# Kernel tuning notes

Hardware: AMD Instinct MI355X
Metric: run time of the kernel (lower is better)

Reference implementation:

```python
import jax, jax.numpy as jnp
import numpy as np

DIM = 128
N = 16          # num_nodes
B = 8           # batch size
H = 4096        # MLP hidden width
SLOPE = 0.01    # LeakyReLU default negative slope
PI_ITERS = 50   # fixed-iteration power iteration (max_error=1e-5 regime)


def setup_inputs() -> dict:
    key = jax.random.key(0)
    ks = jax.random.split(key, 12)
    w = lambda k, shape: jax.random.normal(k, shape, jnp.float32) * 0.02
    return {
        "nodes_embeddings": jax.random.normal(ks[0], (B, N, DIM), jnp.float32),
        "graphs_embeddings": jax.random.normal(ks[1], (B, DIM), jnp.float32),
        "Ts": jax.random.uniform(ks[2], (B, N, N), jnp.float32),
        "W1": w(ks[3], (2 * DIM, H)), "b1": jnp.zeros((H,), jnp.float32),
        "W2": w(ks[4], (H, H)),       "b2": jnp.zeros((H,), jnp.float32),
        "W3": w(ks[5], (H, H)),       "b3": jnp.zeros((H,), jnp.float32),
        "W4": w(ks[6], (H, N * N)),   "b4": jnp.zeros((N * N,), jnp.float32),
    }


def _mlp(x, W1, b1, W2, b2, W3, b3, W4, b4):
    # Linear -> LeakyReLU -> (Dropout=eval identity), x3, then Linear -> LeakyReLU -> Sigmoid
    h = jax.nn.leaky_relu(x @ W1 + b1, SLOPE)
    h = jax.nn.leaky_relu(h @ W2 + b2, SLOPE)
    h = jax.nn.leaky_relu(h @ W3 + b3, SLOPE)
    return jax.nn.sigmoid(jax.nn.leaky_relu(h @ W4 + b4, SLOPE))


def _power_iteration(A):
    # A: (..., n, n), entries > 0 (sigmoid outputs) -> dominant (Perron) eigenvector.
    v0 = jnp.ones(A.shape[:-1], A.dtype)
    def step(v, _):
        w = jnp.einsum('...ij,...j->...i', A, v)
        v = w / jnp.linalg.norm(w, axis=-1, keepdims=True)
        return v, None
    v, _ = jax.lax.scan(step, v0, None, length=PI_ITERS)
    return v


def reference(nodes_embeddings, graphs_embeddings, Ts, W1, b1, W2, b2, W3, b3, W4, b4):
    Bn, Nn, D = nodes_embeddings.shape
    P = Nn * Nn
    pair = jnp.arange(P)
    s_ids = pair // Nn  # outer loop index s
    t_ids = pair % Nn   # inner loop index t

    embT = jnp.transpose(nodes_embeddings, (1, 0, 2))      # (N, B, D)
    s_all = embT[s_ids]                                    # (P, B, D)
    t_all = embT[t_ids]                                    # (P, B, D)
    # Faithful to torch.stack([s, t]).view(batch, 2*dim): a flat reinterpretation,
    # NOT a per-row concat. stack axis=1 -> (P, 2, B, D) then reshape -> (P, B, 2D).
    x = jnp.stack([s_all, t_all], axis=1).reshape(P, Bn, 2 * D)

    pol = _mlp(x.reshape(P * Bn, 2 * D), W1, b1, W2, b2, W3, b3, W4, b4)
    pol = pol.reshape(P, Bn, Nn, Nn)                       # predecessor prob matrices

    vec = _power_iteration(pol)                            # (P, B, N)
    v_src = vec[pair, :, s_ids]                            # (P, B) eigenvector[src]
    T_pair = jnp.transpose(Ts.reshape(Bn, P), (1, 0))      # (P, B), pair order s*N+t

    contrib = vec / v_src[:, :, None] * T_pair[:, :, None]  # (P, B, N)
    return jnp.sum(contrib, axis=0)                         # (B, N) == Cs
```

## Files before the change

kernel.cpp:

```cpp
#include <hip/hip_runtime.h>

typedef unsigned short u16;
typedef unsigned int u32;
typedef __attribute__((ext_vector_type(8))) short short8;
typedef __attribute__((ext_vector_type(4))) float f32x4;

__device__ __forceinline__ u16 f2bf(float f) {
    unsigned u = __float_as_uint(f);
    return (u16)((u + 0x7FFFu + ((u >> 16) & 1u)) >> 16);
}
__device__ __forceinline__ u32 pack2(float a, float b) {
    return ((u32)f2bf(b) << 16) | (u32)f2bf(a);
}

#define ROR1 0x121
#define ROR2 0x122
#define ROR4 0x124
#define ROR8 0x128
template<int C> __device__ __forceinline__ float dppf(float x) {
    int i = __float_as_int(x);
    return __int_as_float(__builtin_amdgcn_update_dpp(i, i, C, 0xF, 0xF, false));
}
template<int C> __device__ __forceinline__ int dppi(int x) {
    return __builtin_amdgcn_update_dpp(x, x, C, 0xF, 0xF, false);
}

template<int SRC, int EPI>
__global__ __launch_bounds__(256, 1) void k_gemm(
    const u16* __restrict__ A, const float* __restrict__ emb,
    const float* __restrict__ W, const float* __restrict__ bias,
    float* __restrict__ Cp, u16* __restrict__ Ho, float* __restrict__ Po,
    int N, int kchunk)
{
    __shared__ __align__(16) u16 Alds[64][40];
    __shared__ __align__(16) u32 Wlds[16 * 132];
    int tid = threadIdx.x;
    int wv = tid >> 6, lane = tid & 63, c = lane & 15, g = lane >> 4;
    int c0 = blockIdx.x * 128;
    int k0 = blockIdx.y * kchunk;
    int nit = kchunk >> 5;

    int ar = tid >> 2, aseg = tid & 3;
    int kp = tid >> 4, cbase = (tid & 15) * 8;

    f32x4 acc[8];
    #pragma unroll
    for (int n = 0; n < 8; ++n) acc[n] = (f32x4){0.f, 0.f, 0.f, 0.f};

    uint4 av;
    float4 q0, q1, q2, q3;

    {
        if (SRC == 0) {
            av = *(const uint4*)(A + (size_t)ar * 4096 + k0 + aseg * 8);
        } else {
            int e0 = aseg * 8;
            int b = 2 * (ar & 3) + (e0 >> 7), d = e0 & 127;
            const float4* s = (const float4*)(emb + (b * 16 + (ar >> 2)) * 128 + d);
            float4 f0 = s[0], f1 = s[1];
            av.x = pack2(f0.x, f0.y); av.y = pack2(f0.z, f0.w);
            av.z = pack2(f1.x, f1.y); av.w = pack2(f1.z, f1.w);
        }
        const float* s0 = W + (size_t)(k0 + 2 * kp) * N + c0 + cbase;
        q0 = ((const float4*)s0)[0]; q1 = ((const float4*)s0)[1];
        const float* s1 = s0 + N;
        q2 = ((const float4*)s1)[0]; q3 = ((const float4*)s1)[1];
    }

    for (int it = 0; it < nit; ++it) {
        *(uint4*)&Alds[ar][aseg * 8] = av;
        {
            uint4 w0, w1;
            w0.x = pack2(q0.x, q2.x); w0.y = pack2(q0.y, q2.y);
            w0.z = pack2(q0.z, q2.z); w0.w = pack2(q0.w, q2.w);
            w1.x = pack2(q1.x, q3.x); w1.y = pack2(q1.y, q3.y);
            w1.z = pack2(q1.z, q3.z); w1.w = pack2(q1.w, q3.w);
            uint4* wd = (uint4*)&Wlds[kp * 132 + cbase];
            wd[0] = w0; wd[1] = w1;
        }
        __syncthreads();

        if (it + 1 < nit) {
            int kc = (it + 1) * 32;
            if (SRC == 0) {
                av = *(const uint4*)(A + (size_t)ar * 4096 + k0 + kc + aseg * 8);
            } else {
                int e0 = kc + aseg * 8;
                int b = 2 * (ar & 3) + (e0 >> 7), d = e0 & 127;
                const float4* s = (const float4*)(emb + (b * 16 + (ar >> 2)) * 128 + d);
                float4 f0 = s[0], f1 = s[1];
                av.x = pack2(f0.x, f0.y); av.y = pack2(f0.z, f0.w);
                av.z = pack2(f1.x, f1.y); av.w = pack2(f1.z, f1.w);
            }
            const float* s0 = W + (size_t)(k0 + kc + 2 * kp) * N + c0 + cbase;
            q0 = ((const float4*)s0)[0]; q1 = ((const float4*)s0)[1];
            const float* s1 = s0 + N;
            q2 = ((const float4*)s1)[0]; q3 = ((const float4*)s1)[1];
        }

        short8 a8 = *(const short8*)&Alds[wv * 16 + c][g * 8];
        #pragma unroll
        for (int n = 0; n < 8; ++n) {
            int base = n * 16 + c;
            union { u32 u[4]; short8 s; } bb;
            bb.u[0] = Wlds[(g * 4 + 0) * 132 + base];
            bb.u[1] = Wlds[(g * 4 + 1) * 132 + base];
            bb.u[2] = Wlds[(g * 4 + 2) * 132 + base];
            bb.u[3] = Wlds[(g * 4 + 3) * 132 + base];
            acc[n] = __builtin_amdgcn_mfma_f32_16x16x32_bf16(a8, bb.s, acc[n], 0, 0, 0);
        }
        __syncthreads();
    }

    #pragma unroll
    for (int n = 0; n < 8; ++n) {
        #pragma unroll
        for (int rr = 0; rr < 4; ++rr) {
            int grow = wv * 16 + g * 4 + rr;
            int gcol = c0 + n * 16 + c;
            float v = acc[n][rr];
            if (EPI == 0) {
                Cp[(size_t)blockIdx.y * 64 * N + (size_t)grow * N + gcol] = v;
            } else {
                v += bias[gcol];
                v = (v >= 0.f) ? v : 0.01f * v;
                if (EPI == 1) Ho[(size_t)grow * N + gcol] = f2bf(v);
                else          Po[(size_t)grow * N + gcol] = 1.0f / (1.0f + __expf(-v));
            }
        }
    }
}

__global__ void k_reduce(const float* __restrict__ Cp, const float* __restrict__ bias,
                         u16* __restrict__ Hb, float* __restrict__ Pf,
                         int N, int ksplit, int mode)
{
    int idx = blockIdx.x * 256 + threadIdx.x;
    int col = idx & (N - 1);
    float s = bias[col];
    for (int k = 0; k < ksplit; ++k) s += Cp[(size_t)k * 64 * N + idx];
    float a = (s >= 0.f) ? s : 0.01f * s;
    if (mode == 0) Hb[idx] = f2bf(a);
    else           Pf[idx] = 1.0f / (1.0f + __expf(-a));
}

__global__ __launch_bounds__(1024) void k_power_out(
    const float* __restrict__ pol,
    const float* __restrict__ Ts,
    float* __restrict__ out)
{
    __shared__ float pol_lds[16384];
    __shared__ float w_lds[64][16];
    __shared__ float Ts_lds[2048];
    __shared__ float Cmat[8][16];

    int tid = threadIdx.x;
    int m = tid >> 4, r = tid & 15;

    {
        const float4* p4 = (const float4*)(pol + tid * 16);
        float4* q4 = (float4*)&pol_lds[tid * 16];
        q4[0] = p4[0]; q4[1] = p4[1]; q4[2] = p4[2]; q4[3] = p4[3];
    }
    Ts_lds[tid] = Ts[tid];
    Ts_lds[tid + 1024] = Ts[tid + 1024];
    __syncthreads();

    float Mr[8], Ms[8];
    {
        int mb = m * 256 + r * 16;
        int idx = r;
        #pragma unroll
        for (int k = 0; k < 8; ++k) { Mr[k] = pol_lds[mb + idx]; idx = dppi<ROR1>(idx); }
        #pragma unroll
        for (int k = 0; k < 8; ++k) { Ms[k] = pol_lds[mb + idx]; idx = dppi<ROR1>(idx); }
    }

    float v = 1.0f;
    #pragma unroll 1
    for (int it = 0; it < 50; ++it) {
        float va = v, vb = dppf<ROR8>(v);
        float w = 0.f, w2 = 0.f;
        #pragma unroll
        for (int k = 0; k < 8; ++k) {
            w  = fmaf(Mr[k], va, w);
            w2 = fmaf(Ms[k], vb, w2);
            if (k < 7) { va = dppf<ROR1>(va); vb = dppf<ROR1>(vb); }
        }
        w += w2;
        if ((it & 7) == 7) {
            float s = w;
            s += dppf<ROR8>(s); s += dppf<ROR4>(s);
            s += dppf<ROR2>(s); s += dppf<ROR1>(s);
            w *= 1.0f / s;
        }
        v = w;
    }
    w_lds[m][r] = v;
    __syncthreads();

    if (tid < 128) {
        int b = tid >> 4, x = tid & 15;
        float s = 0.f;
        if (b < 4) {
            const float* row = &Ts_lds[(b * 16 + x) * 16];
            #pragma unroll
            for (int t = 0; t < 16; ++t) s += row[t];
        } else {
            int j = b - 4;
            #pragma unroll
            for (int si = 0; si < 16; ++si)
                s += Ts_lds[(b * 16 + si) * 16 + x] / w_lds[x * 4 + j][si];
        }
        Cmat[b][x] = s;
    }
    __syncthreads();

    if (tid < 128) {
        int b = tid >> 4, n = tid & 15;
        float o = 0.f;
        if (b < 4) {
            #pragma unroll
            for (int si = 0; si < 16; ++si) {
                const float* wr = w_lds[si * 4 + b];
                o += wr[n] / wr[si] * Cmat[b][si];
            }
        } else {
            int j = b - 4;
            #pragma unroll
            for (int t = 0; t < 16; ++t)
                o += w_lds[t * 4 + j][n] * Cmat[b][t];
        }
        out[b * 16 + n] = o;
    }
}

extern "C" void kernel_launch(void* const* d_in, const int* in_sizes, int n_in,
                              void* d_out, int out_size, void* d_ws, size_t ws_size,
                              hipStream_t stream)
{
    const float* emb = (const float*)d_in[0];
    const float* Ts  = (const float*)d_in[2];
    const float* W1  = (const float*)d_in[3];  const float* b1 = (const float*)d_in[4];
    const float* W2  = (const float*)d_in[5];  const float* b2 = (const float*)d_in[6];
    const float* W3  = (const float*)d_in[7];  const float* b3 = (const float*)d_in[8];
    const float* W4  = (const float*)d_in[9];  const float* b4 = (const float*)d_in[10];
    float* outp = (float*)d_out;

    char* ws = (char*)d_ws;
    u16*   Ha  = (u16*)(ws + 0);
    u16*   Hb  = (u16*)(ws + 524288);
    float* pol = (float*)(ws + 1048576);
    float* Cp  = (float*)(ws + 1114112);

    k_gemm<1, 1><<<dim3(32, 1), 256, 0, stream>>>(
        nullptr, emb, W1, b1, nullptr, Ha, nullptr, 4096, 256);

    k_gemm<0, 0><<<dim3(32, 8), 256, 0, stream>>>(
        Ha, nullptr, W2, nullptr, Cp, nullptr, nullptr, 4096, 512);
    k_reduce<<<1024, 256, 0, stream>>>(Cp, b2, Hb, nullptr, 4096, 8, 0);

    k_gemm<0, 0><<<dim3(32, 8), 256, 0, stream>>>(
        Hb, nullptr, W3, nullptr, Cp, nullptr, nullptr, 4096, 512);
    k_reduce<<<1024, 256, 0, stream>>>(Cp, b3, Ha, nullptr, 4096, 8, 0);

    k_gemm<0, 0><<<dim3(2, 32), 256, 0, stream>>>(
        Ha, nullptr, W4, nullptr, Cp, nullptr, nullptr, 256, 128);
    k_reduce<<<64, 256, 0, stream>>>(Cp, b4, nullptr, pol, 256, 32, 1);

    k_power_out<<<1, 1024, 0, stream>>>(pol, Ts, outp);

    (void)in_sizes; (void)n_in; (void)out_size; (void)ws_size;
}
```

Measured before the change: 85.79 us.

## Double-buffer GEMM global prefetch and raise split-K to sixteen chunks

Rewrites the GEMM main loop into a two-deep register prefetch (A and B sets), so loads for step it+2 are in flight while step it computes. It also relaxes launch bounds to allow two blocks per CU and doubles the split-K factor for the two 4096x4096 layers when the workspace is large enough, giving 512 blocks instead of 256. The goal is better memory latency hiding and more parallelism on the bandwidth-bound weight streaming. The cost is more registers, a larger partial-sum buffer and extra reduce traffic. The loop assumes nit is even.

```diff
diff --git a/kernel.cpp b/kernel.cpp
--- a/kernel.cpp
+++ b/kernel.cpp
@@ -26,7 +26,7 @@
 }
 
 template<int SRC, int EPI>
-__global__ __launch_bounds__(256, 1) void k_gemm(
+__global__ __launch_bounds__(256, 2) void k_gemm(
     const u16* __restrict__ A, const float* __restrict__ emb,
     const float* __restrict__ W, const float* __restrict__ bias,
     float* __restrict__ Cp, u16* __restrict__ Ho, float* __restrict__ Po,
@@ -47,57 +47,36 @@
     #pragma unroll
     for (int n = 0; n < 8; ++n) acc[n] = (f32x4){0.f, 0.f, 0.f, 0.f};
 
-    uint4 av;
-    float4 q0, q1, q2, q3;
-
-    {
+    auto loadA = [&](int kc, uint4& av) {
         if (SRC == 0) {
-            av = *(const uint4*)(A + (size_t)ar * 4096 + k0 + aseg * 8);
+            av = *(const uint4*)(A + (size_t)ar * 4096 + k0 + kc + aseg * 8);
         } else {
-            int e0 = aseg * 8;
+            int e0 = kc + aseg * 8;
             int b = 2 * (ar & 3) + (e0 >> 7), d = e0 & 127;
             const float4* s = (const float4*)(emb + (b * 16 + (ar >> 2)) * 128 + d);
             float4 f0 = s[0], f1 = s[1];
             av.x = pack2(f0.x, f0.y); av.y = pack2(f0.z, f0.w);
             av.z = pack2(f1.x, f1.y); av.w = pack2(f1.z, f1.w);
         }
-        const float* s0 = W + (size_t)(k0 + 2 * kp) * N + c0 + cbase;
+    };
+    auto loadW = [&](int kc, float4& q0, float4& q1, float4& q2, float4& q3) {
+        const float* s0 = W + (size_t)(k0 + kc + 2 * kp) * N + c0 + cbase;
         q0 = ((const float4*)s0)[0]; q1 = ((const float4*)s0)[1];
         const float* s1 = s0 + N;
         q2 = ((const float4*)s1)[0]; q3 = ((const float4*)s1)[1];
-    }
-
-    for (int it = 0; it < nit; ++it) {
+    };
+    auto stage = [&](const uint4& av, const float4& q0, const float4& q1,
+                     const float4& q2, const float4& q3) {
         *(uint4*)&Alds[ar][aseg * 8] = av;
-        {
-            uint4 w0, w1;
-            w0.x = pack2(q0.x, q2.x); w0.y = pack2(q0.y, q2.y);
-            w0.z = pack2(q0.z, q2.z); w0.w = pack2(q0.w, q2.w);
-            w1.x = pack2(q1.x, q3.x); w1.y = pack2(q1.y, q3.y);
-            w1.z = pack2(q1.z, q3.z); w1.w = pack2(q1.w, q3.w);
-            uint4* wd = (uint4*)&Wlds[kp * 132 + cbase];
-            wd[0] = w0; wd[1] = w1;
-        }
-        __syncthreads();
-
-        if (it + 1 < nit) {
-            int kc = (it + 1) * 32;
-            if (SRC == 0) {
-                av = *(const uint4*)(A + (size_t)ar * 4096 + k0 + kc + aseg * 8);
-            } else {
-                int e0 = kc + aseg * 8;
-                int b = 2 * (ar & 3) + (e0 >> 7), d = e0 & 127;
-                const float4* s = (const float4*)(emb + (b * 16 + (ar >> 2)) * 128 + d);
-                float4 f0 = s[0], f1 = s[1];
-                av.x = pack2(f0.x, f0.y); av.y = pack2(f0.z, f0.w);
-                av.z = pack2(f1.x, f1.y); av.w = pack2(f1.z, f1.w);
-            }
-            const float* s0 = W + (size_t)(k0 + kc + 2 * kp) * N + c0 + cbase;
-            q0 = ((const float4*)s0)[0]; q1 = ((const float4*)s0)[1];
-            const float* s1 = s0 + N;
-            q2 = ((const float4*)s1)[0]; q3 = ((const float4*)s1)[1];
-        }
-
+        uint4 w0, w1;
+        w0.x = pack2(q0.x, q2.x); w0.y = pack2(q0.y, q2.y);
+        w0.z = pack2(q0.z, q2.z); w0.w = pack2(q0.w, q2.w);
+        w1.x = pack2(q1.x, q3.x); w1.y = pack2(q1.y, q3.y);
+        w1.z = pack2(q1.z, q3.z); w1.w = pack2(q1.w, q3.w);
+        uint4* wd = (uint4*)&Wlds[kp * 132 + cbase];
+        wd[0] = w0; wd[1] = w1;
+    };
+    auto compute = [&]() {
         short8 a8 = *(const short8*)&Alds[wv * 16 + c][g * 8];
         #pragma unroll
         for (int n = 0; n < 8; ++n) {
@@ -109,6 +88,30 @@
             bb.u[3] = Wlds[(g * 4 + 3) * 132 + base];
             acc[n] = __builtin_amdgcn_mfma_f32_16x16x32_bf16(a8, bb.s, acc[n], 0, 0, 0);
         }
+    };
+
+    uint4 avA, avB;
+    float4 qA0, qA1, qA2, qA3, qB0, qB1, qB2, qB3;
+    loadA(0, avA);  loadW(0, qA0, qA1, qA2, qA3);
+    loadA(32, avB); loadW(32, qB0, qB1, qB2, qB3);
+
+    for (int it = 0; it < nit; it += 2) {
+        stage(avA, qA0, qA1, qA2, qA3);
+        __syncthreads();
+        if (it + 2 < nit) {
+            loadA((it + 2) * 32, avA);
+            loadW((it + 2) * 32, qA0, qA1, qA2, qA3);
+        }
+        compute();
+        __syncthreads();
+
+        stage(avB, qB0, qB1, qB2, qB3);
+        __syncthreads();
+        if (it + 3 < nit) {
+            loadA((it + 3) * 32, avB);
+            loadW((it + 3) * 32, qB0, qB1, qB2, qB3);
+        }
+        compute();
         __syncthreads();
     }
 
@@ -138,6 +141,7 @@
     int idx = blockIdx.x * 256 + threadIdx.x;
     int col = idx & (N - 1);
     float s = bias[col];
+    #pragma unroll 4
     for (int k = 0; k < ksplit; ++k) s += Cp[(size_t)k * 64 * N + idx];
     float a = (s >= 0.f) ? s : 0.01f * s;
     if (mode == 0) Hb[idx] = f2bf(a);
@@ -253,16 +257,20 @@
     float* pol = (float*)(ws + 1048576);
     float* Cp  = (float*)(ws + 1114112);
 
+    size_t need16 = (size_t)1114112 + (size_t)16 * 1048576;
+    int KS = (ws_size >= need16) ? 16 : 8;
+    int kchunk = 4096 / KS;
+
     k_gemm<1, 1><<<dim3(32, 1), 256, 0, stream>>>(
         nullptr, emb, W1, b1, nullptr, Ha, nullptr, 4096, 256);
 
-    k_gemm<0, 0><<<dim3(32, 8), 256, 0, stream>>>(
-        Ha, nullptr, W2, nullptr, Cp, nullptr, nullptr, 4096, 512);
-    k_reduce<<<1024, 256, 0, stream>>>(Cp, b2, Hb, nullptr, 4096, 8, 0);
-
-    k_gemm<0, 0><<<dim3(32, 8), 256, 0, stream>>>(
-        Hb, nullptr, W3, nullptr, Cp, nullptr, nullptr, 4096, 512);
-    k_reduce<<<1024, 256, 0, stream>>>(Cp, b3, Ha, nullptr, 4096, 8, 0);
+    k_gemm<0, 0><<<dim3(32, KS), 256, 0, stream>>>(
+        Ha, nullptr, W2, nullptr, Cp, nullptr, nullptr, 4096, kchunk);
+    k_reduce<<<1024, 256, 0, stream>>>(Cp, b2, Hb, nullptr, 4096, KS, 0);
+
+    k_gemm<0, 0><<<dim3(32, KS), 256, 0, stream>>>(
+        Hb, nullptr, W3, nullptr, Cp, nullptr, nullptr, 4096, kchunk);
+    k_reduce<<<1024, 256, 0, stream>>>(Cp, b3, Ha, nullptr, 4096, KS, 0);
 
     k_gemm<0, 0><<<dim3(2, 32), 256, 0, stream>>>(
         Ha, nullptr, W4, nullptr, Cp, nullptr, nullptr, 256, 128);
```

New measurement: 79.62 us. 1.08x faster.
